# Optimization experiments

Measured on AMD Instinct MI355X. Metric: run time of the kernel, lower is better.

Reference implementation:

```python
import jax, jax.numpy as jnp
import numpy as np

B, S, D, H = 2, 2048, 1024, 16
DEPTH = D // H

def setup_inputs() -> dict:
    key = jax.random.key(0)
    ks = jax.random.split(key, 6)
    sc = 0.02
    return {
        "x": jax.random.normal(ks[0], (B, S, D), dtype=jnp.float32),
        "mask": jnp.ones((S, S), dtype=jnp.int32),
        "wq": jax.random.normal(ks[1], (D, D), dtype=jnp.float32) * sc,
        "bq": jnp.zeros((D,), dtype=jnp.float32),
        "wk": jax.random.normal(ks[2], (D, D), dtype=jnp.float32) * sc,
        "bk": jnp.zeros((D,), dtype=jnp.float32),
        "wv": jax.random.normal(ks[3], (D, D), dtype=jnp.float32) * sc,
        "bv": jnp.zeros((D,), dtype=jnp.float32),
        "wo": jax.random.normal(ks[4], (D, D), dtype=jnp.float32) * sc,
        "bo": jnp.zeros((D,), dtype=jnp.float32),
    }

def _split_heads(t):
    # [B,S,D] -> [B,H,S,depth]
    b, s, _ = t.shape
    return t.reshape(b, s, H, DEPTH).transpose(0, 2, 1, 3)

def reference(x, mask, wq, bq, wk, bk, wv, bv, wo, bo):
    q = _split_heads(x @ wq + bq)
    k = _split_heads(x @ wk + bk)
    v = _split_heads(x @ wv + bv)
    scale = 1.0 / jnp.sqrt(jnp.asarray(DEPTH, x.dtype))
    scores = jnp.einsum('bhqd,bhkd->bhqk', q, k) * scale
    # Faithful to original: band_part(ones,-1,0) is the LOWER triangle
    # (incl. diagonal), and it is ADDED times -1e9 -> lower triangle masked.
    s_len = mask.shape[0]
    tri = jnp.tril(jnp.ones((s_len, s_len), dtype=x.dtype))
    scores = scores + tri * (-1e9)
    attn = jax.nn.softmax(scores, axis=-1)  # dropout is identity at inference
    out = jnp.einsum('bhqk,bhkd->bhqd', attn, v)
    out = out.transpose(0, 2, 1, 3).reshape(x.shape[0], -1, D)
    return out @ wo + bo
```

## Files before the change

### kernel.cpp

```cpp
#include <hip/hip_runtime.h>
#include <hip/hip_bf16.h>


using bf16   = __bf16;
using bf16x2 = __attribute__((ext_vector_type(2))) __bf16;
using bf16x4 = __attribute__((ext_vector_type(4))) __bf16;
using bf16x8 = __attribute__((ext_vector_type(8))) __bf16;
using f32x4  = __attribute__((ext_vector_type(4))) float;
using uintx2 = __attribute__((ext_vector_type(2))) unsigned int;
using uintx4 = __attribute__((ext_vector_type(4))) unsigned int;

#define ATTN_LOG2E 1.4426950408889634f
#define ATTN_MBIAS (-11.541560327111707f)

__device__ __forceinline__ void load_lds16(const void* g, void* l) {
  __builtin_amdgcn_global_load_lds(
      (const __attribute__((address_space(1))) void*)g,
      (__attribute__((address_space(3))) void*)l, 16, 0, 0);
}

__device__ __forceinline__ unsigned int packbf(float a, float b) {
  bf16x2 v;
  v[0] = (bf16)a;
  v[1] = (bf16)b;
  return __builtin_bit_cast(unsigned int, v);
}

__device__ __forceinline__ void xchg_p(unsigned int u, unsigned int v, int hi,
                                       unsigned int& f, unsigned int& s) {
#if __has_builtin(__builtin_amdgcn_permlane32_swap) && \
    __has_builtin(__builtin_amdgcn_permlane16_swap)
  uintx2 ab = __builtin_amdgcn_permlane32_swap(u, v, false, false);
  uintx2 fs = __builtin_amdgcn_permlane16_swap(ab[0], ab[1], false, false);
  f = fs[0];
  s = fs[1];
#else
  unsigned int a = (hi < 2) ? u : (unsigned int)__shfl_xor((int)v, 32);
  unsigned int b = (hi < 2) ? (unsigned int)__shfl_xor((int)u, 32) : v;
  unsigned int a16 = (unsigned int)__shfl_xor((int)a, 16);
  unsigned int b16 = (unsigned int)__shfl_xor((int)b, 16);
  f = (hi & 1) ? b16 : a;
  s = (hi & 1) ? b : a16;
#endif
}

__device__ const unsigned int kChunkTab[36] = {
    0u  | (0u << 8)  | (11u << 16) | (0u << 24),
    0u  | (11u << 8) | (22u << 16) | (1u << 24),
    0u  | (22u << 8) | (32u << 16) | (2u << 24),
    1u  | (2u << 8)  | (12u << 16) | (0u << 24),
    1u  | (12u << 8) | (22u << 16) | (1u << 24),
    1u  | (22u << 8) | (32u << 16) | (2u << 24),
    2u  | (4u << 8)  | (14u << 16) | (0u << 24),
    2u  | (14u << 8) | (23u << 16) | (1u << 24),
    2u  | (23u << 8) | (32u << 16) | (2u << 24),
    3u  | (6u << 8)  | (15u << 16) | (0u << 24),
    3u  | (15u << 8) | (24u << 16) | (1u << 24),
    4u  | (8u << 8)  | (16u << 16) | (0u << 24),
    4u  | (16u << 8) | (24u << 16) | (1u << 24),
    4u  | (24u << 8) | (32u << 16) | (2u << 24),
    8u  | (16u << 8) | (24u << 16) | (0u << 24),
    8u  | (24u << 8) | (32u << 16) | (1u << 24),
    12u | (24u << 8) | (32u << 16) | (3u << 24),
    3u  | (24u << 8) | (32u << 16) | (2u << 24),
    5u  | (10u << 8) | (18u << 16) | (0u << 24),
    5u  | (18u << 8) | (25u << 16) | (1u << 24),
    5u  | (25u << 8) | (32u << 16) | (2u << 24),
    6u  | (12u << 8) | (19u << 16) | (0u << 24),
    6u  | (19u << 8) | (26u << 16) | (1u << 24),
    9u  | (18u << 8) | (25u << 16) | (0u << 24),
    9u  | (25u << 8) | (32u << 16) | (1u << 24),
    6u  | (26u << 8) | (32u << 16) | (2u << 24),
    7u  | (14u << 8) | (20u << 16) | (0u << 24),
    7u  | (20u << 8) | (26u << 16) | (1u << 24),
    7u  | (26u << 8) | (32u << 16) | (2u << 24),
    10u | (20u << 8) | (26u << 16) | (0u << 24),
    10u | (26u << 8) | (32u << 16) | (1u << 24),
    13u | (26u << 8) | (32u << 16) | (3u << 24),
    11u | (22u << 8) | (27u << 16) | (0u << 24),
    11u | (27u << 8) | (32u << 16) | (1u << 24),
    14u | (28u << 8) | (32u << 16) | (3u << 24),
    15u | (30u << 8) | (32u << 16) | (3u << 24)};

__global__ __launch_bounds__(256) void prep_kernel(
    const float* __restrict__ x, bf16* __restrict__ xb,
    const float* __restrict__ wq, const float* __restrict__ wk,
    const float* __restrict__ wv, const float* __restrict__ wo,
    bf16* __restrict__ wT) {
  const int t = threadIdx.x;
  int bid = blockIdx.x;
  if (bid < 4096) {
    const int i = (bid * 256 + t) * 4;
    const float4 v = *(const float4*)(x + i);
    bf16x4 o;
    o[0] = (bf16)v.x; o[1] = (bf16)v.y; o[2] = (bf16)v.z; o[3] = (bf16)v.w;
    *(bf16x4*)(xb + i) = o;
    return;
  }
  bid -= 4096;
  const int sel = bid >> 8;
  const float* w = (sel == 0) ? wq : (sel == 1) ? wk : (sel == 2) ? wv : wo;
  bf16* out = wT + (size_t)sel * 1048576;
  __shared__ float tile[64][65];
  const int n0 = (bid & 15) * 64;
  const int k0 = ((bid >> 4) & 15) * 64;
#pragma unroll
  for (int p = 0; p < 4; ++p) {
    const int row = p * 16 + (t >> 4);
    const int c4  = (t & 15) * 4;
    const float4 v = *(const float4*)&w[(size_t)(k0 + row) * 1024 + n0 + c4];
    tile[row][c4 + 0] = v.x; tile[row][c4 + 1] = v.y;
    tile[row][c4 + 2] = v.z; tile[row][c4 + 3] = v.w;
  }
  __syncthreads();
#pragma unroll
  for (int p = 0; p < 4; ++p) {
    const int rn = p * 16 + (t >> 4);
    const int c4 = (t & 15) * 4;
    bf16x4 o;
#pragma unroll
    for (int j = 0; j < 4; ++j) o[j] = (bf16)tile[c4 + j][rn];
    *(bf16x4*)&out[(size_t)(n0 + rn) * 1024 + k0 + c4] = o;
  }
}

__global__ __launch_bounds__(256, 2) void gemm_qkv(
    const bf16* __restrict__ A, const bf16* __restrict__ Bt,
    const float* __restrict__ bias0, const float* __restrict__ bias1,
    const float* __restrict__ bias2, bf16* __restrict__ qf,
    bf16* __restrict__ kfr, bf16* __restrict__ vfr) {
  __shared__ __align__(16) char smem[40960];
  char* sA = smem;
  char* sB = smem + 16384;
  const int tid = threadIdx.x;
  const int lane = tid & 63;
  const int qlo = lane & 15;
  const int hi = lane >> 4;
  const int w = tid >> 6;
  const int wm = w >> 1, wn = w & 1;
  const int bid = blockIdx.x;
  const int m0 = (bid >> 4) * 128;
  const int n0 = (bid & 15) * 192;

  const char* Ab = (const char*)A;
  const char* Bb = (const char*)Bt;
  const int r_ = tid >> 3;
  size_t srcA[4], srcB[6];
#pragma unroll
  for (int i = 0; i < 4; ++i) {
    const int r = i * 32 + r_;
    const int cg = (tid & 7) ^ (r & 7);
    srcA[i] = (size_t)(m0 + r) * 2048 + cg * 16;
  }
#pragma unroll
  for (int i = 0; i < 6; ++i) {
    const int r = i * 32 + r_;
    const int cg = (tid & 7) ^ (r & 7);
    srcB[i] = (size_t)(n0 + r) * 2048 + cg * 16;
  }

  f32x4 acc[4][6] = {};

  for (int kt = 0; kt < 16; ++kt) {
    const size_t kb = (size_t)kt * 128;
#pragma unroll
    for (int i = 0; i < 4; ++i)
      load_lds16(Ab + srcA[i] + kb, sA + i * 4096 + tid * 16);
#pragma unroll
    for (int i = 0; i < 6; ++i)
      load_lds16(Bb + srcB[i] + kb, sB + i * 4096 + tid * 16);
    asm volatile("s_waitcnt vmcnt(0)" ::: "memory");
    __syncthreads();
#pragma unroll
    for (int ks = 0; ks < 2; ++ks) {
      const int g = hi + 4 * ks;
      bf16x8 aF[4], bF[6];
#pragma unroll
      for (int mi = 0; mi < 4; ++mi) {
        const int ra = wm * 64 + mi * 16 + qlo;
        aF[mi] = *(const bf16x8*)(sA + ra * 128 + ((g ^ (ra & 7)) << 4));
      }
#pragma unroll
      for (int ni = 0; ni < 6; ++ni) {
        const int rb = wn * 96 + ni * 16 + qlo;
        bF[ni] = *(const bf16x8*)(sB + rb * 128 + ((g ^ (rb & 7)) << 4));
      }
#pragma unroll
      for (int mi = 0; mi < 4; ++mi)
#pragma unroll
        for (int ni = 0; ni < 6; ++ni)
          acc[mi][ni] = __builtin_amdgcn_mfma_f32_16x16x32_bf16(
              aF[mi], bF[ni], acc[mi][ni], 0, 0, 0);
    }
    __syncthreads();
  }

#pragma unroll
  for (int mi = 0; mi < 4; ++mi) {
#pragma unroll
    for (int ni = 0; ni < 6; ++ni) {
      const int n  = n0 + wn * 96 + ni * 16 + qlo;
      const int mb = m0 + wm * 64 + mi * 16 + 4 * hi;
      const f32x4 v = acc[mi][ni];
      const float bias =
          (n < 1024) ? bias0[n] : ((n < 2048) ? bias1[n - 1024] : bias2[n - 2048]);
      if (n < 1024) {
#pragma unroll
        for (int j = 0; j < 4; ++j)
          qf[(size_t)(mb + j) * 1024 + n] = (bf16)(v[j] + bias);
      } else if (n < 2048) {
        const int dg = n - 1024;
        const int hh = dg >> 6, d = dg & 63;
        const int ks = d >> 5, hl = (d >> 3) & 3, e = d & 7;
        const int bb = mb >> 11, sl = mb & 2047;
        const int ktt = sl >> 6, tt = (sl >> 4) & 3, ql = sl & 15;
        bf16* dst = kfr +
                    ((((size_t)(bb * 16 + hh) * 32 + ktt) * 4 + tt) * 2 + ks) *
                        512 +
                    (hl * 16 + ql) * 8 + e;
#pragma unroll
        for (int j = 0; j < 4; ++j) dst[j * 8] = (bf16)(v[j] + bias);
      } else {
        const int dg = n - 2048;
        const int hh = dg >> 6, d = dg & 63;
        const int dt = d >> 4, dc = d & 15;
        const int bb = mb >> 11, sl = mb & 2047;
        const int ktt = sl >> 6, ks = (sl >> 5) & 1, hl = (sl >> 3) & 3,
                  e0 = sl & 7;
        bf16x4 pk;
#pragma unroll
        for (int j = 0; j < 4; ++j) pk[j] = (bf16)(v[j] + bias);
        *(bf16x4*)(vfr +
                   ((((size_t)(bb * 16 + hh) * 32 + ktt) * 4 + dt) * 2 + ks) *
                       512 +
                   (hl * 16 + dc) * 8 + e0) = pk;
      }
    }
  }
}

__global__ __launch_bounds__(256, 2) void gemm_out(
    const bf16* __restrict__ A, const bf16* __restrict__ Bt,
    const float* __restrict__ bias0, float* __restrict__ fout) {
  __shared__ __align__(16) char smem[24576];
  char* sA = smem;
  char* sB = smem + 8192;
  const int tid = threadIdx.x;
  const int lane = tid & 63;
  const int qlo = lane & 15;
  const int hi = lane >> 4;
  const int w = tid >> 6;
  const int wm = w >> 1, wn = w & 1;
  const int bid = blockIdx.x;
  const int m0 = (bid >> 3) * 64;
  const int n0 = (bid & 7) * 128;

  const char* Ab = (const char*)A;
  const char* Bb = (const char*)Bt;
  const int r_ = tid >> 3;
  size_t srcA[2], srcB[4];
#pragma unroll
  for (int i = 0; i < 2; ++i) {
    const int r = r_ + i * 32;
    const int cg = (tid & 7) ^ (r & 7);
    srcA[i] = (size_t)(m0 + r) * 2048 + cg * 16;
  }
#pragma unroll
  for (int i = 0; i < 4; ++i) {
    const int r = r_ + i * 32;
    const int cg = (tid & 7) ^ (r & 7);
    srcB[i] = (size_t)(n0 + r) * 2048 + cg * 16;
  }

  f32x4 acc[2][4] = {};

  for (int kt = 0; kt < 16; ++kt) {
    const size_t kb = (size_t)kt * 128;
#pragma unroll
    for (int i = 0; i < 2; ++i)
      load_lds16(Ab + srcA[i] + kb, sA + i * 4096 + tid * 16);
#pragma unroll
    for (int i = 0; i < 4; ++i)
      load_lds16(Bb + srcB[i] + kb, sB + i * 4096 + tid * 16);
    asm volatile("s_waitcnt vmcnt(0)" ::: "memory");
    __syncthreads();
#pragma unroll
    for (int ks = 0; ks < 2; ++ks) {
      const int g = hi + 4 * ks;
      bf16x8 aF[2], bF[4];
#pragma unroll
      for (int mi = 0; mi < 2; ++mi) {
        const int ra = wm * 32 + mi * 16 + qlo;
        aF[mi] = *(const bf16x8*)(sA + ra * 128 + ((g ^ (ra & 7)) << 4));
      }
#pragma unroll
      for (int ni = 0; ni < 4; ++ni) {
        const int rb = wn * 64 + ni * 16 + qlo;
        bF[ni] = *(const bf16x8*)(sB + rb * 128 + ((g ^ (rb & 7)) << 4));
      }
#pragma unroll
      for (int mi = 0; mi < 2; ++mi)
#pragma unroll
        for (int ni = 0; ni < 4; ++ni)
          acc[mi][ni] = __builtin_amdgcn_mfma_f32_16x16x32_bf16(
              aF[mi], bF[ni], acc[mi][ni], 0, 0, 0);
    }
    __syncthreads();
  }

#pragma unroll
  for (int mi = 0; mi < 2; ++mi) {
#pragma unroll
    for (int ni = 0; ni < 4; ++ni) {
      const int n  = n0 + wn * 64 + ni * 16 + qlo;
      const int mb = m0 + wm * 32 + mi * 16 + 4 * hi;
      const f32x4 v = acc[mi][ni];
      const float bias = bias0[n];
#pragma unroll
      for (int j = 0; j < 4; ++j)
        fout[(size_t)(mb + j) * 1024 + n] = v[j] + bias;
    }
  }
}

__global__ __launch_bounds__(256, 2) void attn_kernel(
    const bf16* __restrict__ qf, const bf16* __restrict__ kfr,
    const bf16* __restrict__ vfr, bf16* __restrict__ ao,
    bf16* __restrict__ sc1, bf16* __restrict__ sc2,
    float* __restrict__ lbuf) {
  const int tid  = threadIdx.x;
  const int lane = tid & 63;
  const int hi   = lane >> 4;
  const int qlo  = lane & 15;
  const int w    = tid >> 6;
  const int u  = blockIdx.x >> 5;
  const int bh = blockIdx.x & 31;
  const int b = bh >> 4, h = bh & 15;

  const unsigned int ent = kChunkTab[u];
  const int jq = ent & 255, kbeg = (ent >> 8) & 255, kend = (ent >> 16) & 255;
  const int slot = ent >> 24;

  const char* kfb = (const char*)kfr + (size_t)bh * 262144 + lane * 16;
  const char* vfb = (const char*)vfr + (size_t)bh * 262144 + lane * 16;
  const char* qbb = (const char*)qf + ((size_t)b * 2048) * 2048 + h * 128;

  bf16x8 onesB;
#pragma unroll
  for (int i = 0; i < 8; ++i) onesB[i] = (bf16)1.0f;

  const int q0 = jq * 128;
  const int qb = q0 + w * 32;

  bf16x8 qA[2][2];
#pragma unroll
  for (int nt = 0; nt < 2; ++nt) {
    const char* qrow = qbb + (size_t)(qb + 16 * nt + qlo) * 2048;
#pragma unroll
    for (int ks = 0; ks < 2; ++ks) {
      qA[nt][ks] = *(const bf16x8*)(qrow + ks * 64 + hi * 16);
#pragma unroll
      for (int i = 0; i < 8; ++i)
        qA[nt][ks][i] = (bf16)(0.125f * (float)qA[nt][ks][i]);
    }
  }

  f32x4 lacc[2] = {};
  f32x4 O[2][4] = {};

  for (int kt = kbeg; kt < kend; ++kt) {
    const char* kT = kfb + (size_t)kt * 8192;
    const char* vT = vfb + (size_t)kt * 8192;
    bf16x8 kFr[2][4], vF[2][4];
#pragma unroll
    for (int ks = 0; ks < 2; ++ks)
#pragma unroll
      for (int t = 0; t < 4; ++t)
        kFr[ks][t] = *(const bf16x8*)(kT + (t * 2 + ks) * 1024);
#pragma unroll
    for (int ks = 0; ks < 2; ++ks)
#pragma unroll
      for (int dt = 0; dt < 4; ++dt)
        vF[ks][dt] = *(const bf16x8*)(vT + (dt * 2 + ks) * 1024);

    f32x4 sc[2][4] = {};
#pragma unroll
    for (int ks = 0; ks < 2; ++ks)
#pragma unroll
      for (int t = 0; t < 4; ++t) {
        sc[0][t] = __builtin_amdgcn_mfma_f32_16x16x32_bf16(
            kFr[ks][t], qA[0][ks], sc[0][t], 0, 0, 0);
        sc[1][t] = __builtin_amdgcn_mfma_f32_16x16x32_bf16(
            kFr[ks][t], qA[1][ks], sc[1][t], 0, 0, 0);
      }

    if (kt * 64 < q0 + 128) {
      const int k0t = kt * 64;
#pragma unroll
      for (int nt = 0; nt < 2; ++nt)
#pragma unroll
        for (int t = 0; t < 4; ++t)
#pragma unroll
          for (int j = 0; j < 4; ++j) {
            const int kk = k0t + t * 16 + 4 * hi + j;
            const int qq = qb + 16 * nt + qlo;
            if (kk <= qq) sc[nt][t][j] = -1e30f;
          }
    }

#pragma unroll
    for (int nt = 0; nt < 2; ++nt) {
      unsigned int W[4][2];
#pragma unroll
      for (int t = 0; t < 4; ++t)
#pragma unroll
        for (int p = 0; p < 2; ++p)
          W[t][p] = packbf(
              exp2f(fmaf(sc[nt][t][2 * p], ATTN_LOG2E, ATTN_MBIAS)),
              exp2f(fmaf(sc[nt][t][2 * p + 1], ATTN_LOG2E, ATTN_MBIAS)));
#pragma unroll
      for (int ks = 0; ks < 2; ++ks) {
        uintx4 w4;
#pragma unroll
        for (int p = 0; p < 2; ++p) {
          unsigned int f, s;
          xchg_p(W[2 * ks][p], W[2 * ks + 1][p], hi, f, s);
          w4[p] = f;
          w4[2 + p] = s;
        }
        const bf16x8 pA = __builtin_bit_cast(bf16x8, w4);
        lacc[nt] = __builtin_amdgcn_mfma_f32_16x16x32_bf16(pA, onesB, lacc[nt],
                                                           0, 0, 0);
#pragma unroll
        for (int dt = 0; dt < 4; ++dt)
          O[nt][dt] = __builtin_amdgcn_mfma_f32_16x16x32_bf16(
              pA, vF[ks][dt], O[nt][dt], 0, 0, 0);
      }
    }
  }

  if (slot == 3) {
#pragma unroll
    for (int nt = 0; nt < 2; ++nt)
#pragma unroll
      for (int j = 0; j < 4; ++j) {
        const float linv = (lacc[nt][j] > 0.f) ? 1.f / lacc[nt][j] : 0.f;
        const int qg = qb + 16 * nt + 4 * hi + j;
#pragma unroll
        for (int dt = 0; dt < 4; ++dt)
          ao[(size_t)(b * 2048 + qg) * 1024 + h * 64 + dt * 16 + qlo] =
              (bf16)(O[nt][dt][j] * linv);
      }
  } else {
    const int qtbh = jq * 32 + bh;
#pragma unroll
    for (int nt = 0; nt < 2; ++nt)
#pragma unroll
      for (int j = 0; j < 4; ++j) {
        const int r = w * 32 + 16 * nt + 4 * hi + j;
#pragma unroll
        for (int dt = 0; dt < 4; ++dt) {
          const bf16 vv = (bf16)O[nt][dt][j];
          if (slot == 0)
            ao[(size_t)(b * 2048 + q0 + r) * 1024 + h * 64 + dt * 16 + qlo] =
                vv;
          else {
            bf16* sc_ = (slot == 1) ? sc1 : sc2;
            sc_[(size_t)(qtbh * 128 + r) * 64 + dt * 16 + qlo] = vv;
          }
        }
      }
    if (qlo == 0) {
#pragma unroll
      for (int nt = 0; nt < 2; ++nt)
#pragma unroll
        for (int j = 0; j < 4; ++j)
          lbuf[slot * 49152 + qtbh * 128 + (w * 32 + 16 * nt + 4 * hi + j)] =
              lacc[nt][j];
    }
  }
}

__global__ __launch_bounds__(256) void combine_kernel(
    const bf16* __restrict__ sc1, const bf16* __restrict__ sc2,
    const float* __restrict__ lbuf, const bf16* __restrict__ vfr,
    bf16* __restrict__ ao) {
  const int bid = blockIdx.x;
  if (bid >= 384) {
    const int tid = threadIdx.x;
    const int lane = tid & 63, w = tid >> 6;
    const int gw = (bid - 384) * 4 + w;
    const int bh = gw >> 2, dt = gw & 3;
    const int b = bh >> 4, h = bh & 15;
    const char* vfb = (const char*)vfr + (size_t)bh * 262144 + lane * 16;
    float s = 0.f;
    for (int kt = 0; kt < 32; ++kt) {
#pragma unroll
      for (int ks = 0; ks < 2; ++ks) {
        const bf16x8 v =
            *(const bf16x8*)(vfb + (size_t)kt * 8192 + (dt * 2 + ks) * 1024);
#pragma unroll
        for (int e = 0; e < 8; ++e) s += (float)v[e];
      }
    }
    s += __shfl_xor(s, 16);
    s += __shfl_xor(s, 32);
    if ((lane >> 4) == 0)
      ao[(size_t)(b * 2048 + 2047) * 1024 + h * 64 + dt * 16 + lane] =
          (bf16)(s * (1.f / 2048.f));
    return;
  }

  const int qtbh = bid;
  const int jq = qtbh >> 5, bh = qtbh & 31;
  const int b = bh >> 4, h = bh & 15;
  const int t = threadIdx.x;
  const int r = t >> 1;
  const int c0 = (t & 1) * 32;
  const bool three = (jq < 8);

  float l = lbuf[qtbh * 128 + r] + lbuf[49152 + qtbh * 128 + r];
  if (three) l += lbuf[98304 + qtbh * 128 + r];
  const float linv = (l > 0.f) ? 1.f / l : 0.f;

  bf16* arow = ao + ((size_t)(b * 2048 + jq * 128 + r) * 1024 + h * 64 + c0);
  const bf16* s1row = sc1 + ((size_t)(qtbh * 128 + r) * 64 + c0);
  const bf16* s2row = sc2 + ((size_t)(qtbh * 128 + r) * 64 + c0);
#pragma unroll
  for (int i = 0; i < 4; ++i) {
    const bf16x8 o0 = *(const bf16x8*)(arow + i * 8);
    const bf16x8 o1 = *(const bf16x8*)(s1row + i * 8);
    bf16x8 o2;
    if (three) o2 = *(const bf16x8*)(s2row + i * 8);
    bf16x8 o;
#pragma unroll
    for (int j = 0; j < 8; ++j) {
      float acc = (float)o0[j] + (float)o1[j];
      if (three) acc += (float)o2[j];
      o[j] = (bf16)(acc * linv);
    }
    *(bf16x8*)(arow + i * 8) = o;
  }
}

extern "C" void kernel_launch(void* const* d_in, const int* in_sizes, int n_in,
                              void* d_out, int out_size, void* d_ws,
                              size_t ws_size, hipStream_t stream) {
  const float* x  = (const float*)d_in[0];
  const float* wq = (const float*)d_in[2];
  const float* bq = (const float*)d_in[3];
  const float* wk = (const float*)d_in[4];
  const float* bk = (const float*)d_in[5];
  const float* wv = (const float*)d_in[6];
  const float* bv = (const float*)d_in[7];
  const float* wo = (const float*)d_in[8];
  const float* bo = (const float*)d_in[9];
  float* out = (float*)d_out;

  if (ws_size < (size_t)25165824 * 2) return;

  bf16* ws    = (bf16*)d_ws;
  bf16* xb    = ws;
  bf16* wqkvT = xb + 4194304;
  bf16* woT   = wqkvT + 3145728;
  bf16* qfp   = woT + 1048576;
  bf16* kfrag = qfp + 4194304;
  bf16* vfrag = kfrag + 4194304;
  bf16* aop   = vfrag + 4194304;

  bf16*  sc1  = xb;
  float* lbuf = (float*)(xb + 3145728);
  bf16*  sc2  = wqkvT;

  prep_kernel<<<5120, 256, 0, stream>>>(x, xb, wq, wk, wv, wo, wqkvT);

  gemm_qkv<<<512, 256, 0, stream>>>(xb, wqkvT, bq, bk, bv, qfp, kfrag, vfrag);
  attn_kernel<<<1152, 256, 0, stream>>>(qfp, kfrag, vfrag, aop, sc1, sc2, lbuf);
  combine_kernel<<<416, 256, 0, stream>>>(sc1, sc2, lbuf, vfrag, aop);
  gemm_out<<<512, 256, 0, stream>>>(aop, woT, bo, out);
}
```

Baseline: 105.3 us.

## Double-buffer LDS tiles in QKV and output projection GEMMs

Both projection GEMMs now use two LDS buffers and issue the next k-tile's global-to-LDS loads before computing on the current tile. This hides global load latency behind the MFMA work and drops one barrier per iteration. The cost is twice the shared memory per block (80 KB for gemm_qkv), which may limit how many blocks fit per CU under launch_bounds(256,2).

```diff
diff --git a/kernel.cpp b/kernel.cpp
--- a/kernel.cpp
+++ b/kernel.cpp
@@ -129,9 +129,7 @@
     const float* __restrict__ bias0, const float* __restrict__ bias1,
     const float* __restrict__ bias2, bf16* __restrict__ qf,
     bf16* __restrict__ kfr, bf16* __restrict__ vfr) {
-  __shared__ __align__(16) char smem[40960];
-  char* sA = smem;
-  char* sB = smem + 16384;
+  __shared__ __align__(16) char smem[81920];
   const int tid = threadIdx.x;
   const int lane = tid & 63;
   const int qlo = lane & 15;
@@ -161,16 +159,28 @@
 
   f32x4 acc[4][6] = {};
 
+  auto STAGE = [&](int kt, int buf) {
+    const size_t kb = (size_t)kt * 128;
+    char* dA = smem + buf * 40960;
+    char* dB = dA + 16384;
+#pragma unroll
+    for (int i = 0; i < 4; ++i)
+      load_lds16(Ab + srcA[i] + kb, dA + i * 4096 + tid * 16);
+#pragma unroll
+    for (int i = 0; i < 6; ++i)
+      load_lds16(Bb + srcB[i] + kb, dB + i * 4096 + tid * 16);
+  };
+
+  STAGE(0, 0);
+  asm volatile("s_waitcnt vmcnt(0)" ::: "memory");
+  __syncthreads();
+
   for (int kt = 0; kt < 16; ++kt) {
-    const size_t kb = (size_t)kt * 128;
-#pragma unroll
-    for (int i = 0; i < 4; ++i)
-      load_lds16(Ab + srcA[i] + kb, sA + i * 4096 + tid * 16);
-#pragma unroll
-    for (int i = 0; i < 6; ++i)
-      load_lds16(Bb + srcB[i] + kb, sB + i * 4096 + tid * 16);
-    asm volatile("s_waitcnt vmcnt(0)" ::: "memory");
-    __syncthreads();
+    const int cur = kt & 1;
+    if (kt + 1 < 16) STAGE(kt + 1, cur ^ 1);
+
+    const char* sA = smem + cur * 40960;
+    const char* sB = sA + 16384;
 #pragma unroll
     for (int ks = 0; ks < 2; ++ks) {
       const int g = hi + 4 * ks;
@@ -192,7 +202,10 @@
           acc[mi][ni] = __builtin_amdgcn_mfma_f32_16x16x32_bf16(
               aF[mi], bF[ni], acc[mi][ni], 0, 0, 0);
     }
-    __syncthreads();
+    if (kt + 1 < 16) {
+      asm volatile("s_waitcnt vmcnt(0)" ::: "memory");
+      __syncthreads();
+    }
   }
 
 #pragma unroll
@@ -242,9 +255,7 @@
 __global__ __launch_bounds__(256, 2) void gemm_out(
     const bf16* __restrict__ A, const bf16* __restrict__ Bt,
     const float* __restrict__ bias0, float* __restrict__ fout) {
-  __shared__ __align__(16) char smem[24576];
-  char* sA = smem;
-  char* sB = smem + 8192;
+  __shared__ __align__(16) char smem[49152];
   const int tid = threadIdx.x;
   const int lane = tid & 63;
   const int qlo = lane & 15;
@@ -274,16 +285,28 @@
 
   f32x4 acc[2][4] = {};
 
+  auto STAGE = [&](int kt, int buf) {
+    const size_t kb = (size_t)kt * 128;
+    char* dA = smem + buf * 24576;
+    char* dB = dA + 8192;
+#pragma unroll
+    for (int i = 0; i < 2; ++i)
+      load_lds16(Ab + srcA[i] + kb, dA + i * 4096 + tid * 16);
+#pragma unroll
+    for (int i = 0; i < 4; ++i)
+      load_lds16(Bb + srcB[i] + kb, dB + i * 4096 + tid * 16);
+  };
+
+  STAGE(0, 0);
+  asm volatile("s_waitcnt vmcnt(0)" ::: "memory");
+  __syncthreads();
+
   for (int kt = 0; kt < 16; ++kt) {
-    const size_t kb = (size_t)kt * 128;
-#pragma unroll
-    for (int i = 0; i < 2; ++i)
-      load_lds16(Ab + srcA[i] + kb, sA + i * 4096 + tid * 16);
-#pragma unroll
-    for (int i = 0; i < 4; ++i)
-      load_lds16(Bb + srcB[i] + kb, sB + i * 4096 + tid * 16);
-    asm volatile("s_waitcnt vmcnt(0)" ::: "memory");
-    __syncthreads();
+    const int cur = kt & 1;
+    if (kt + 1 < 16) STAGE(kt + 1, cur ^ 1);
+
+    const char* sA = smem + cur * 24576;
+    const char* sB = sA + 8192;
 #pragma unroll
     for (int ks = 0; ks < 2; ++ks) {
       const int g = hi + 4 * ks;
@@ -305,7 +328,10 @@
           acc[mi][ni] = __builtin_amdgcn_mfma_f32_16x16x32_bf16(
               aF[mi], bF[ni], acc[mi][ni], 0, 0, 0);
     }
-    __syncthreads();
+    if (kt + 1 < 16) {
+      asm volatile("s_waitcnt vmcnt(0)" ::: "memory");
+      __syncthreads();
+    }
   }
 
 #pragma unroll
```

New measurement: 103.3 us, median of 2. Within noise of the previous version (-1.9%).
